# Performance work log

Hardware: AMD Instinct MI355X
Metric: run time of the kernel (lower is better)

The kernel has to match this reference:

```python
import jax, jax.numpy as jnp
import numpy as np

TOPK = 2
NORM_TOPK = True
SCALE = 1.0
EPS = 1e-9


def setup_inputs() -> dict:
    key = jax.random.key(0)
    ks = jax.random.split(key, 9)
    h, i, E = 2048, 1024, 16
    std = 0.02
    return {
        "x": jax.random.normal(ks[0], (1, 2048, h), jnp.float32),
        "Wr": jax.random.normal(ks[1], (E, h), jnp.float32) * std,
        "bias": jnp.zeros((E,), jnp.float32),
        "Wg": jax.random.normal(ks[2], (E, h, i), jnp.float32) * std,
        "Wu": jax.random.normal(ks[3], (E, h, i), jnp.float32) * std,
        "Wd": jax.random.normal(ks[4], (E, i, h), jnp.float32) * std,
        "sWg": jax.random.normal(ks[5], (h, i), jnp.float32) * std,
        "sWu": jax.random.normal(ks[6], (h, i), jnp.float32) * std,
        "sWd": jax.random.normal(ks[7], (i, h), jnp.float32) * std,
    }


def reference(x, Wr, bias, Wg, Wu, Wd, sWg, sWu, sWd):
    b, s, h = x.shape
    E = Wr.shape[0]
    xt = x.reshape(b * s, h)  # [T, h]

    # Router: softmax over expert logits, then top-k
    logits = xt @ Wr.T + bias  # [T, E]
    probs = jax.nn.softmax(logits, axis=-1)
    topk_val, topk_idx = jax.lax.top_k(probs, TOPK)  # [T, K]
    if NORM_TOPK:
        w = topk_val / (jnp.sum(topk_val, axis=-1, keepdims=True) + EPS)
    else:
        w = topk_val
    w = w * SCALE

    # Dense per-expert SwiGLU (mathematically identical to gather/scatter dispatch)
    g = jnp.einsum('th,ehi->tei', xt, Wg)  # [T, E, i]
    u = jnp.einsum('th,ehi->tei', xt, Wu)
    y = jnp.einsum('tei,eih->teh', jax.nn.silu(g) * u, Wd)  # [T, E, h]

    # Combine: out[t] = sum_k w[t,k] * y[t, idx[t,k]]
    oh = jax.nn.one_hot(topk_idx, E, dtype=x.dtype)  # [T, K, E]
    routed = jnp.einsum('tke,tk,teh->th', oh, w, y)

    # Shared expert (SwiGLU)
    shared = (jax.nn.silu(xt @ sWg) * (xt @ sWu)) @ sWd

    return (routed + shared).reshape(b, s, h)
```

## Files before the change

### kernel.cpp

```cpp
#include <hip/hip_runtime.h>
#include <hip/hip_bf16.h>

#define T_TOK 2048
#define HDIM  2048
#define IDIM  1024
#define NE    16
#define NEX   17
#define NASSIGN (T_TOK*3)
#define TM    64

#define G1_NCT 16
#define G2_NCT 32
#define G1_NWG (TM*G1_NCT)
#define G2_NWG (TM*G2_NCT)

typedef __attribute__((ext_vector_type(8))) short bf16x8;
typedef __attribute__((ext_vector_type(4))) float f32x4;

#define WAITVM(N) asm volatile("s_waitcnt vmcnt(" #N ")" ::: "memory")
#define WAITLGKM  asm volatile("s_waitcnt lgkmcnt(0)" ::: "memory")
#define SCHEDB    __builtin_amdgcn_sched_barrier(0)
#define BARRIER   __builtin_amdgcn_s_barrier()

__device__ __forceinline__ unsigned short f2bf(float f) {
    union { float f; unsigned u; } v; v.f = f;
    unsigned r = v.u + 0x7fffu + ((v.u >> 16) & 1u);
    return (unsigned short)(r >> 16);
}
__device__ __forceinline__ unsigned pack2f(float a, float b) {
    __hip_bfloat162 h = __float22bfloat162_rn(float2{a, b});
    unsigned r;
    __builtin_memcpy(&r, &h, 4);
    return r;
}
__device__ __forceinline__ float fidx(const float4& v, int j) {
    return ((const float*)&v)[j];
}
__device__ __forceinline__ int SW(int r) { return (r ^ (r >> 2)) & 7; }
__device__ __forceinline__ int lds_off(int row, int kelem) {
    return (row << 7) + ((((kelem >> 3) ^ SW(row))) << 4) + ((kelem & 7) << 1);
}
__device__ __forceinline__ f32x4 mfma16(bf16x8 a, bf16x8 b, f32x4 c) {
    return __builtin_amdgcn_mfma_f32_16x16x32_bf16(a, b, c, 0, 0, 0);
}
__device__ __forceinline__ void gload_lds16(const void* g, void* lds) {
    __builtin_amdgcn_global_load_lds(
        (const __attribute__((address_space(1))) unsigned*)g,
        (__attribute__((address_space(3))) unsigned*)lds, 16, 0, 0);
}

__global__ __launch_bounds__(256) void k_cvt(const float* __restrict__ x,
                                             unsigned short* __restrict__ xbf) {
    int i = blockIdx.x * 256 + threadIdx.x;
    float4 v = ((const float4*)x)[i];
    uint2 p{pack2f(v.x, v.y), pack2f(v.z, v.w)};
    ((uint2*)xbf)[i] = p;
}

__global__ void k_router(const float* __restrict__ x, const float* __restrict__ Wr,
                         const float* __restrict__ bias, float* __restrict__ wtok,
                         int* __restrict__ idxtok, int* __restrict__ counts) {
    int t = blockIdx.x;
    int lane = threadIdx.x & 63;
    int wave = threadIdx.x >> 6;
    __shared__ float lg[NE];
    const float4* xr = (const float4*)(x + (size_t)t * HDIM);
    for (int e = wave; e < NE; e += 4) {
        const float4* wr = (const float4*)(Wr + (size_t)e * HDIM);
        float s = 0.f;
        for (int j = lane; j < HDIM / 4; j += 64) {
            float4 a = xr[j], b = wr[j];
            s += a.x*b.x + a.y*b.y + a.z*b.z + a.w*b.w;
        }
        #pragma unroll
        for (int d = 32; d; d >>= 1) s += __shfl_xor(s, d);
        if (lane == 0) lg[e] = s + bias[e];
    }
    __syncthreads();
    if (threadIdx.x == 0) {
        float m = lg[0];
        #pragma unroll
        for (int e = 1; e < NE; e++) m = fmaxf(m, lg[e]);
        float p[NE]; float S = 0.f;
        #pragma unroll
        for (int e = 0; e < NE; e++) { p[e] = expf(lg[e] - m); S += p[e]; }
        int i0 = 0;
        #pragma unroll
        for (int e = 1; e < NE; e++) if (p[e] > p[i0]) i0 = e;
        int i1 = (i0 == 0) ? 1 : 0;
        for (int e = 0; e < NE; e++) if (e != i0 && p[e] > p[i1]) i1 = e;
        float v0 = p[i0] / S, v1 = p[i1] / S;
        float wsum = v0 + v1 + 1e-9f;
        wtok[t*2+0] = v0 / wsum;
        wtok[t*2+1] = v1 / wsum;
        idxtok[t*2+0] = i0;
        idxtok[t*2+1] = i1;
        atomicAdd(&counts[i0], 1);
        atomicAdd(&counts[i1], 1);
    }
}

__global__ void k_scan(const int* __restrict__ counts, int* __restrict__ offs,
                       int* __restrict__ cursor, int4* __restrict__ tiles) {
    if (threadIdx.x == 0) {
        int acc = 0;
        for (int e = 0; e < NEX; e++) {
            offs[e] = acc; cursor[e] = acc;
            acc += (e < NE) ? counts[e] : T_TOK;
        }
        offs[NEX] = acc;
        int nt = 0;
        for (int e = 0; e < NEX; e++) {
            for (int r = offs[e]; r < offs[e+1]; r += 128) {
                tiles[nt] = int4{r, min(128, offs[e+1] - r), e, 0};
                nt++;
            }
        }
        for (; nt < TM; nt++) tiles[nt] = int4{0, 0, 0, 0};
    }
}

__global__ void k_scatter(const int* __restrict__ idxtok, const float* __restrict__ wtok,
                          int* __restrict__ cursor, const int* __restrict__ offs,
                          int* __restrict__ rows, float* __restrict__ wrow) {
    int t = blockIdx.x * blockDim.x + threadIdx.x;
    if (t >= T_TOK) return;
    #pragma unroll
    for (int k = 0; k < 2; k++) {
        int e = idxtok[t*2+k];
        int pos = atomicAdd(&cursor[e], 1);
        rows[pos] = t;
        wrow[pos] = wtok[t*2+k];
    }
    int p16 = offs[NE] + t;
    rows[p16] = t;
    wrow[p16] = 1.0f;
}

__global__ __launch_bounds__(512) void k_gemm1(
        const unsigned short* __restrict__ xbf,
        const float* __restrict__ Wg, const float* __restrict__ Wu,
        const float* __restrict__ sWg, const float* __restrict__ sWu,
        const int4* __restrict__ tiles, const int* __restrict__ rows,
        const float* __restrict__ wrow, unsigned short* __restrict__ act) {
    int bid = blockIdx.x;
    int wg = (bid & 7) * (G1_NWG >> 3) + (bid >> 3);
    int ti = wg & (TM - 1);
    int ct = wg >> 6;

    int4 tl = tiles[ti];
    int nrows = tl.y;
    if (nrows == 0) return;
    int rs = tl.x, e = tl.z;
    const float* wgp = (e < NE) ? Wg + (size_t)e * HDIM * IDIM : sWg;
    const float* wup = (e < NE) ? Wu + (size_t)e * HDIM * IDIM : sWu;
    int n0 = ct * 64;

    __shared__ unsigned short As[2][128 * 64];
    __shared__ unsigned short Bs[2][64 * 64];
    __shared__ unsigned short Us[2][64 * 64];
    __shared__ int rloc[128];

    int tid = threadIdx.x;
    if (tid < 128) rloc[tid] = rows[rs + min(tid, nrows - 1)];
    __syncthreads();

    int l = tid & 63, w = tid >> 6;
    int ar0 = w * 8 + (l >> 3);
    int ar1 = 64 + ar0;
    const unsigned short* asrc0 = xbf + (size_t)rloc[ar0] * HDIM + (((l & 7) ^ SW(ar0)) << 3);
    const unsigned short* asrc1 = xbf + (size_t)rloc[ar1] * HDIM + (((l & 7) ^ SW(ar1)) << 3);

    int n4 = (tid & 15) << 2;
    int kb = (tid >> 4) << 1;
    const float* gsrc = wgp + (size_t)kb * IDIM + n0 + n4;
    const float* usrc = wup + (size_t)kb * IDIM + n0 + n4;

    int wr = (w >> 2) << 6;
    int wc = (w & 3) << 4;
    int fr = l & 15;
    int fk = (l >> 4) << 3;

    float4 gR[2][2], uR[2][2];

    #define G1_LOADW(K0, S) do { \
        gR[S][0] = *(const float4*)(gsrc + (size_t)(K0) * IDIM); \
        gR[S][1] = *(const float4*)(gsrc + (size_t)(K0) * IDIM + IDIM); \
        uR[S][0] = *(const float4*)(usrc + (size_t)(K0) * IDIM); \
        uR[S][1] = *(const float4*)(usrc + (size_t)(K0) * IDIM + IDIM); \
    } while (0)

    #define G1_GLOADA(K0, B) do { \
        gload_lds16(asrc0 + (K0), (char*)As[B] + w * 1024); \
        gload_lds16(asrc1 + (K0), (char*)As[B] + 8192 + w * 1024); \
    } while (0)

    #define G1_WRITEW(S, B) do { \
        _Pragma("unroll") \
        for (int i = 0; i < 4; ++i) { \
            int n = n4 + i; \
            *(unsigned*)((char*)Bs[B] + lds_off(n, kb)) = pack2f(fidx(gR[S][0],i), fidx(gR[S][1],i)); \
            *(unsigned*)((char*)Us[B] + lds_off(n, kb)) = pack2f(fidx(uR[S][0],i), fidx(uR[S][1],i)); \
        } \
    } while (0)

    #define G1_MFMA(B) do { \
        _Pragma("unroll") \
        for (int kh = 0; kh < 2; ++kh) { \
            int kk = (kh << 5) + fk; \
            bf16x8 a[4], bg, bu; \
            _Pragma("unroll") \
            for (int m = 0; m < 4; ++m) \
                a[m] = *(const bf16x8*)((const char*)As[B] + lds_off(wr + m * 16 + fr, kk)); \
            bg = *(const bf16x8*)((const char*)Bs[B] + lds_off(wc + fr, kk)); \
            bu = *(const bf16x8*)((const char*)Us[B] + lds_off(wc + fr, kk)); \
            _Pragma("unroll") \
            for (int m = 0; m < 4; ++m) { \
                accg[m] = mfma16(a[m], bg, accg[m]); \
                accu[m] = mfma16(a[m], bu, accu[m]); \
            } \
        } \
    } while (0)

    #define G1_STEP(K, S, BC, BN) do { \
        G1_GLOADA(min(((K)+1)*64, KLAST), BN); \
        G1_WRITEW(S, BN); \
        G1_LOADW(min(((K)+3)*64, KLAST), S); \
        SCHEDB; \
        G1_MFMA(BC); \
        SCHEDB; \
        WAITVM(4); \
        WAITLGKM; \
        BARRIER; \
    } while (0)

    f32x4 accg[4] = {}, accu[4] = {};
    const int NK = HDIM / 64;
    const int KLAST = (NK - 1) * 64;

    G1_LOADW(0, 0);
    G1_LOADW(64, 1);
    G1_GLOADA(0, 0);
    SCHEDB;
    WAITVM(6);
    G1_WRITEW(0, 0);
    G1_LOADW(128, 0);
    SCHEDB;
    WAITVM(4);
    WAITLGKM;
    BARRIER;

    for (int k = 0; k < NK; k += 2) {
        G1_STEP(k,     1, 0, 1);
        G1_STEP(k + 1, 0, 1, 0);
    }
    WAITVM(0);

    int crow = (l >> 4) << 2;
    int ccol = l & 15;
    #pragma unroll
    for (int m = 0; m < 4; ++m) {
        #pragma unroll
        for (int reg = 0; reg < 4; ++reg) {
            int r = wr + m * 16 + crow + reg;
            if (r < nrows) {
                float wv = wrow[rs + r];
                float g = accg[m][reg], u = accu[m][reg];
                act[(size_t)(rs + r) * IDIM + n0 + wc + ccol] =
                    f2bf(g / (1.f + __expf(-g)) * u * wv);
            }
        }
    }
    #undef G1_LOADW
    #undef G1_GLOADA
    #undef G1_WRITEW
    #undef G1_MFMA
    #undef G1_STEP
}

__global__ __launch_bounds__(512) void k_gemm2(
        const unsigned short* __restrict__ act,
        const float* __restrict__ Wd, const float* __restrict__ sWd,
        const int4* __restrict__ tiles, const int* __restrict__ rows,
        float* __restrict__ out) {
    int bid = blockIdx.x;
    int wg = (bid & 7) * (G2_NWG >> 3) + (bid >> 3);
    int ti = wg & (TM - 1);
    int ct = wg >> 6;

    int4 tl = tiles[ti];
    int nrows = tl.y;
    if (nrows == 0) return;
    int rs = tl.x, e = tl.z;
    const float* wdp = (e < NE) ? Wd + (size_t)e * IDIM * HDIM : sWd;
    int n0 = ct * 64;

    __shared__ unsigned short As[2][128 * 64];
    __shared__ unsigned short Bs[2][64 * 64];
    __shared__ int rloc[128];

    int tid = threadIdx.x;
    if (tid < 128) rloc[tid] = rows[rs + min(tid, nrows - 1)];
    __syncthreads();

    int l = tid & 63, w = tid >> 6;
    int ar0 = w * 8 + (l >> 3);
    int ar1 = 64 + ar0;
    const unsigned short* asrc0 = act + (size_t)(rs + ar0) * IDIM + (((l & 7) ^ SW(ar0)) << 3);
    const unsigned short* asrc1 = act + (size_t)(rs + ar1) * IDIM + (((l & 7) ^ SW(ar1)) << 3);

    int n4 = (tid & 15) << 2;
    int kb = (tid >> 4) << 1;
    const float* dsrc = wdp + (size_t)kb * HDIM + n0 + n4;

    int wr = (w >> 2) << 6;
    int wc = (w & 3) << 4;
    int fr = l & 15;
    int fk = (l >> 4) << 3;

    float4 dR[2][2];

    #define G2_LOADW(K0, S) do { \
        dR[S][0] = *(const float4*)(dsrc + (size_t)(K0) * HDIM); \
        dR[S][1] = *(const float4*)(dsrc + (size_t)(K0) * HDIM + HDIM); \
    } while (0)

    #define G2_GLOADA(K0, B) do { \
        gload_lds16(asrc0 + (K0), (char*)As[B] + w * 1024); \
        gload_lds16(asrc1 + (K0), (char*)As[B] + 8192 + w * 1024); \
    } while (0)

    #define G2_WRITEW(S, B) do { \
        _Pragma("unroll") \
        for (int i = 0; i < 4; ++i) { \
            int n = n4 + i; \
            *(unsigned*)((char*)Bs[B] + lds_off(n, kb)) = pack2f(fidx(dR[S][0],i), fidx(dR[S][1],i)); \
        } \
    } while (0)

    #define G2_MFMA(B) do { \
        _Pragma("unroll") \
        for (int kh = 0; kh < 2; ++kh) { \
            int kk = (kh << 5) + fk; \
            bf16x8 a[4], b; \
            _Pragma("unroll") \
            for (int m = 0; m < 4; ++m) \
                a[m] = *(const bf16x8*)((const char*)As[B] + lds_off(wr + m * 16 + fr, kk)); \
            b = *(const bf16x8*)((const char*)Bs[B] + lds_off(wc + fr, kk)); \
            _Pragma("unroll") \
            for (int m = 0; m < 4; ++m) \
                acc[m] = mfma16(a[m], b, acc[m]); \
        } \
    } while (0)

    #define G2_STEP(K, S, BC, BN) do { \
        G2_GLOADA(min(((K)+1)*64, KLAST), BN); \
        G2_WRITEW(S, BN); \
        G2_LOADW(min(((K)+3)*64, KLAST), S); \
        SCHEDB; \
        G2_MFMA(BC); \
        SCHEDB; \
        WAITVM(2); \
        WAITLGKM; \
        BARRIER; \
    } while (0)

    f32x4 acc[4] = {};
    const int NK = IDIM / 64;
    const int KLAST = (NK - 1) * 64;

    G2_LOADW(0, 0);
    G2_LOADW(64, 1);
    G2_GLOADA(0, 0);
    SCHEDB;
    WAITVM(4);
    G2_WRITEW(0, 0);
    G2_LOADW(128, 0);
    SCHEDB;
    WAITVM(2);
    WAITLGKM;
    BARRIER;

    for (int k = 0; k < NK; k += 2) {
        G2_STEP(k,     1, 0, 1);
        G2_STEP(k + 1, 0, 1, 0);
    }
    WAITVM(0);

    int crow = (l >> 4) << 2;
    int ccol = l & 15;
    #pragma unroll
    for (int m = 0; m < 4; ++m) {
        #pragma unroll
        for (int reg = 0; reg < 4; ++reg) {
            int r = wr + m * 16 + crow + reg;
            if (r < nrows) {
                atomicAdd(&out[(size_t)rloc[r] * HDIM + n0 + wc + ccol], acc[m][reg]);
            }
        }
    }
    #undef G2_LOADW
    #undef G2_GLOADA
    #undef G2_WRITEW
    #undef G2_MFMA
    #undef G2_STEP
}

extern "C" void kernel_launch(void* const* d_in, const int* in_sizes, int n_in,
                              void* d_out, int out_size, void* d_ws, size_t ws_size,
                              hipStream_t stream) {
    const float* x    = (const float*)d_in[0];
    const float* Wr   = (const float*)d_in[1];
    const float* bias = (const float*)d_in[2];
    const float* Wg   = (const float*)d_in[3];
    const float* Wu   = (const float*)d_in[4];
    const float* Wd   = (const float*)d_in[5];
    const float* sWg  = (const float*)d_in[6];
    const float* sWu  = (const float*)d_in[7];
    const float* sWd  = (const float*)d_in[8];
    float* out = (float*)d_out;

    char* p = (char*)d_ws;
    int*   counts = (int*)p;                 p += 256;
    int*   offs   = (int*)p;                 p += 256;
    int*   cursor = (int*)p;                 p += 256;
    int4*  tiles  = (int4*)p;                p += TM * sizeof(int4);
    int*   idxtok = (int*)p;                 p += (size_t)T_TOK * 2 * sizeof(int);
    float* wtok   = (float*)p;               p += (size_t)T_TOK * 2 * sizeof(float);
    int*   rows   = (int*)p;                 p += (size_t)NASSIGN * sizeof(int);
    float* wrow   = (float*)p;               p += (size_t)NASSIGN * sizeof(float);
    unsigned short* act = (unsigned short*)p; p += (size_t)NASSIGN * IDIM * sizeof(unsigned short);
    unsigned short* xbf = (unsigned short*)p;

    hipMemsetAsync(counts, 0, 256, stream);
    hipMemsetAsync(d_out, 0, (size_t)out_size * sizeof(float), stream);

    k_cvt<<<dim3(T_TOK * HDIM / 1024), dim3(256), 0, stream>>>(x, xbf);
    k_router<<<dim3(T_TOK), dim3(256), 0, stream>>>(x, Wr, bias, wtok, idxtok, counts);
    k_scan<<<dim3(1), dim3(64), 0, stream>>>(counts, offs, cursor, tiles);
    k_scatter<<<dim3((T_TOK + 255) / 256), dim3(256), 0, stream>>>(idxtok, wtok, cursor, offs, rows, wrow);
    k_gemm1<<<dim3(G1_NWG), dim3(512), 0, stream>>>(xbf, Wg, Wu, sWg, sWu, tiles, rows, wrow, act);
    k_gemm2<<<dim3(G2_NWG), dim3(512), 0, stream>>>(act, Wd, sWd, tiles, rows, out);
}
```

Measured before the change: 334.1 us.

## Restructure GEMM pipelines: single-buffer B tiles, reorder prefetch, add occupancy hints

```diff
diff --git a/kernel.cpp b/kernel.cpp
--- a/kernel.cpp
+++ b/kernel.cpp
@@ -137,7 +137,7 @@
     wrow[p16] = 1.0f;
 }
 
-__global__ __launch_bounds__(512) void k_gemm1(
+__global__ __launch_bounds__(512, 6) void k_gemm1(
         const unsigned short* __restrict__ xbf,
         const float* __restrict__ Wg, const float* __restrict__ Wu,
         const float* __restrict__ sWg, const float* __restrict__ sWu,
@@ -157,19 +157,17 @@
     int n0 = ct * 64;
 
     __shared__ unsigned short As[2][128 * 64];
-    __shared__ unsigned short Bs[2][64 * 64];
-    __shared__ unsigned short Us[2][64 * 64];
-    __shared__ int rloc[128];
+    __shared__ unsigned short Bs[64 * 64];
+    __shared__ unsigned short Us[64 * 64];
 
     int tid = threadIdx.x;
-    if (tid < 128) rloc[tid] = rows[rs + min(tid, nrows - 1)];
-    __syncthreads();
-
     int l = tid & 63, w = tid >> 6;
     int ar0 = w * 8 + (l >> 3);
     int ar1 = 64 + ar0;
-    const unsigned short* asrc0 = xbf + (size_t)rloc[ar0] * HDIM + (((l & 7) ^ SW(ar0)) << 3);
-    const unsigned short* asrc1 = xbf + (size_t)rloc[ar1] * HDIM + (((l & 7) ^ SW(ar1)) << 3);
+    int rr0 = rows[rs + min(ar0, nrows - 1)];
+    int rr1 = rows[rs + min(ar1, nrows - 1)];
+    const unsigned short* asrc0 = xbf + (size_t)rr0 * HDIM + (((l & 7) ^ SW(ar0)) << 3);
+    const unsigned short* asrc1 = xbf + (size_t)rr1 * HDIM + (((l & 7) ^ SW(ar1)) << 3);
 
     int n4 = (tid & 15) << 2;
     int kb = (tid >> 4) << 1;
@@ -195,12 +193,12 @@
         gload_lds16(asrc1 + (K0), (char*)As[B] + 8192 + w * 1024); \
     } while (0)
 
-    #define G1_WRITEW(S, B) do { \
+    #define G1_WRITEW(S) do { \
         _Pragma("unroll") \
         for (int i = 0; i < 4; ++i) { \
             int n = n4 + i; \
-            *(unsigned*)((char*)Bs[B] + lds_off(n, kb)) = pack2f(fidx(gR[S][0],i), fidx(gR[S][1],i)); \
-            *(unsigned*)((char*)Us[B] + lds_off(n, kb)) = pack2f(fidx(uR[S][0],i), fidx(uR[S][1],i)); \
+            *(unsigned*)((char*)Bs + lds_off(n, kb)) = pack2f(fidx(gR[S][0],i), fidx(gR[S][1],i)); \
+            *(unsigned*)((char*)Us + lds_off(n, kb)) = pack2f(fidx(uR[S][0],i), fidx(uR[S][1],i)); \
         } \
     } while (0)
 
@@ -212,8 +210,8 @@
             _Pragma("unroll") \
             for (int m = 0; m < 4; ++m) \
                 a[m] = *(const bf16x8*)((const char*)As[B] + lds_off(wr + m * 16 + fr, kk)); \
-            bg = *(const bf16x8*)((const char*)Bs[B] + lds_off(wc + fr, kk)); \
-            bu = *(const bf16x8*)((const char*)Us[B] + lds_off(wc + fr, kk)); \
+            bg = *(const bf16x8*)((const char*)Bs + lds_off(wc + fr, kk)); \
+            bu = *(const bf16x8*)((const char*)Us + lds_off(wc + fr, kk)); \
             _Pragma("unroll") \
             for (int m = 0; m < 4; ++m) { \
                 accg[m] = mfma16(a[m], bg, accg[m]); \
@@ -222,16 +220,19 @@
         } \
     } while (0)
 
-    #define G1_STEP(K, S, BC, BN) do { \
-        G1_GLOADA(min(((K)+1)*64, KLAST), BN); \
-        G1_WRITEW(S, BN); \
-        G1_LOADW(min(((K)+3)*64, KLAST), S); \
-        SCHEDB; \
-        G1_MFMA(BC); \
-        SCHEDB; \
-        WAITVM(4); \
+    #define G1_STEP(K, SB, AB) do { \
+        G1_MFMA(AB); \
+        SCHEDB; \
+        BARRIER; \
+        SCHEDB; \
+        G1_WRITEW(SB); \
+        G1_LOADW(min(((K)+3)*64, KLAST), SB); \
+        G1_GLOADA(min(((K)+2)*64, KLAST), AB); \
+        SCHEDB; \
+        WAITVM(6); \
         WAITLGKM; \
         BARRIER; \
+        SCHEDB; \
     } while (0)
 
     f32x4 accg[4] = {}, accu[4] = {};
@@ -243,16 +244,19 @@
     G1_GLOADA(0, 0);
     SCHEDB;
     WAITVM(6);
-    G1_WRITEW(0, 0);
+    SCHEDB;
+    G1_WRITEW(0);
     G1_LOADW(128, 0);
-    SCHEDB;
-    WAITVM(4);
+    G1_GLOADA(64, 1);
+    SCHEDB;
+    WAITVM(6);
     WAITLGKM;
     BARRIER;
+    SCHEDB;
 
     for (int k = 0; k < NK; k += 2) {
-        G1_STEP(k,     1, 0, 1);
-        G1_STEP(k + 1, 0, 1, 0);
+        G1_STEP(k,     1, 0);
+        G1_STEP(k + 1, 0, 1);
     }
     WAITVM(0);
 
@@ -278,7 +282,7 @@
     #undef G1_STEP
 }
 
-__global__ __launch_bounds__(512) void k_gemm2(
+__global__ __launch_bounds__(512, 8) void k_gemm2(
         const unsigned short* __restrict__ act,
         const float* __restrict__ Wd, const float* __restrict__ sWd,
         const int4* __restrict__ tiles, const int* __restrict__ rows,
@@ -296,18 +300,14 @@
     int n0 = ct * 64;
 
     __shared__ unsigned short As[2][128 * 64];
-    __shared__ unsigned short Bs[2][64 * 64];
-    __shared__ int rloc[128];
+    __shared__ unsigned short Bs[64 * 64];
 
     int tid = threadIdx.x;
-    if (tid < 128) rloc[tid] = rows[rs + min(tid, nrows - 1)];
-    __syncthreads();
-
     int l = tid & 63, w = tid >> 6;
     int ar0 = w * 8 + (l >> 3);
     int ar1 = 64 + ar0;
-    const unsigned short* asrc0 = act + (size_t)(rs + ar0) * IDIM + (((l & 7) ^ SW(ar0)) << 3);
-    const unsigned short* asrc1 = act + (size_t)(rs + ar1) * IDIM + (((l & 7) ^ SW(ar1)) << 3);
+    const unsigned short* asrc0 = act + (size_t)(rs + min(ar0, nrows - 1)) * IDIM + (((l & 7) ^ SW(ar0)) << 3);
+    const unsigned short* asrc1 = act + (size_t)(rs + min(ar1, nrows - 1)) * IDIM + (((l & 7) ^ SW(ar1)) << 3);
 
     int n4 = (tid & 15) << 2;
     int kb = (tid >> 4) << 1;
@@ -330,11 +330,11 @@
         gload_lds16(asrc1 + (K0), (char*)As[B] + 8192 + w * 1024); \
     } while (0)
 
-    #define G2_WRITEW(S, B) do { \
+    #define G2_WRITEW(S) do { \
         _Pragma("unroll") \
         for (int i = 0; i < 4; ++i) { \
             int n = n4 + i; \
-            *(unsigned*)((char*)Bs[B] + lds_off(n, kb)) = pack2f(fidx(dR[S][0],i), fidx(dR[S][1],i)); \
+            *(unsigned*)((char*)Bs + lds_off(n, kb)) = pack2f(fidx(dR[S][0],i), fidx(dR[S][1],i)); \
         } \
     } while (0)
 
@@ -346,23 +346,26 @@
             _Pragma("unroll") \
             for (int m = 0; m < 4; ++m) \
                 a[m] = *(const bf16x8*)((const char*)As[B] + lds_off(wr + m * 16 + fr, kk)); \
-            b = *(const bf16x8*)((const char*)Bs[B] + lds_off(wc + fr, kk)); \
+            b = *(const bf16x8*)((const char*)Bs + lds_off(wc + fr, kk)); \
             _Pragma("unroll") \
             for (int m = 0; m < 4; ++m) \
                 acc[m] = mfma16(a[m], b, acc[m]); \
         } \
     } while (0)
 
-    #define G2_STEP(K, S, BC, BN) do { \
-        G2_GLOADA(min(((K)+1)*64, KLAST), BN); \
-        G2_WRITEW(S, BN); \
-        G2_LOADW(min(((K)+3)*64, KLAST), S); \
-        SCHEDB; \
-        G2_MFMA(BC); \
-        SCHEDB; \
-        WAITVM(2); \
+    #define G2_STEP(K, SB, AB) do { \
+        G2_MFMA(AB); \
+        SCHEDB; \
+        BARRIER; \
+        SCHEDB; \
+        G2_WRITEW(SB); \
+        G2_LOADW(min(((K)+3)*64, KLAST), SB); \
+        G2_GLOADA(min(((K)+2)*64, KLAST), AB); \
+        SCHEDB; \
+        WAITVM(4); \
         WAITLGKM; \
         BARRIER; \
+        SCHEDB; \
     } while (0)
 
     f32x4 acc[4] = {};
@@ -374,16 +377,19 @@
     G2_GLOADA(0, 0);
     SCHEDB;
     WAITVM(4);
-    G2_WRITEW(0, 0);
+    SCHEDB;
+    G2_WRITEW(0);
     G2_LOADW(128, 0);
-    SCHEDB;
-    WAITVM(2);
+    G2_GLOADA(64, 1);
+    SCHEDB;
+    WAITVM(4);
     WAITLGKM;
     BARRIER;
+    SCHEDB;
 
     for (int k = 0; k < NK; k += 2) {
-        G2_STEP(k,     1, 0, 1);
-        G2_STEP(k + 1, 0, 1, 0);
+        G2_STEP(k,     1, 0);
+        G2_STEP(k + 1, 0, 1);
     }
     WAITVM(0);
 
@@ -395,7 +401,7 @@
         for (int reg = 0; reg < 4; ++reg) {
             int r = wr + m * 16 + crow + reg;
             if (r < nrows) {
-                atomicAdd(&out[(size_t)rloc[r] * HDIM + n0 + wc + ccol], acc[m][reg]);
+                atomicAdd(&out[(size_t)rows[rs + r] * HDIM + n0 + wc + ccol], acc[m][reg]);
             }
         }
     }
```

Result: slower. 756.6 us (+126.4%).
